# Kernel optimization log

Hardware: AMD Instinct MI355X
Metric: run time of the kernel (lower is better)

## Reference

```python
import jax, jax.numpy as jnp
import numpy as np

D_MODEL = 1024
H = 16
D_K = D_MODEL // H


def setup_inputs() -> dict:
    key = jax.random.key(0)
    ks = jax.random.split(key, 12)
    B, S = 2, 2048
    inp = {
        "q": jax.random.normal(ks[0], (B, S, D_MODEL), jnp.float32),
        "k": jax.random.normal(ks[1], (B, S, D_MODEL), jnp.float32),
        "v": jax.random.normal(ks[2], (B, S, D_MODEL), jnp.float32),
        "mask": jax.random.randint(ks[3], (1, 1, S, S), 0, 2, jnp.int32),
    }
    s = 1.0 / np.sqrt(D_MODEL)
    inp["wq_w"] = jax.random.normal(ks[4], (D_MODEL, D_MODEL), jnp.float32) * s
    inp["wq_b"] = jnp.zeros((D_MODEL,), jnp.float32)
    inp["wk_w"] = jax.random.normal(ks[5], (D_MODEL, D_MODEL), jnp.float32) * s
    inp["wk_b"] = jnp.zeros((D_MODEL,), jnp.float32)
    inp["wv_w"] = jax.random.normal(ks[6], (D_MODEL, D_MODEL), jnp.float32) * s
    inp["wv_b"] = jnp.zeros((D_MODEL,), jnp.float32)
    inp["wo_w"] = jax.random.normal(ks[7], (D_MODEL, D_MODEL), jnp.float32) * s
    inp["wo_b"] = jnp.zeros((D_MODEL,), jnp.float32)
    return inp


def reference(q, k, v, mask, wq_w, wq_b, wk_w, wk_b, wv_w, wv_b, wo_w, wo_b):
    B, S, _ = q.shape
    # projections (torch Linear: x @ W^T + b)
    def proj(x, w, b):
        y = x @ w.T + b
        return y.reshape(B, S, H, D_K).transpose(0, 2, 1, 3)  # [B,H,S,Dk]

    Q = proj(q, wq_w, wq_b)
    K = proj(k, wk_w, wk_b)
    V = proj(v, wv_w, wv_b)

    scores = jnp.einsum("bhqd,bhkd->bhqk", Q, K) / jnp.sqrt(jnp.float32(D_K))
    # source quirk: masked positions set to 1e-9 (NOT -inf) before softmax
    scores = jnp.where(mask == 0, jnp.float32(1e-9), scores)
    attn = jax.nn.softmax(scores, axis=-1)
    out = jnp.einsum("bhqk,bhkd->bhqd", attn, V)
    out = out.transpose(0, 2, 1, 3).reshape(B, S, H * D_K)
    return out @ wo_w.T + wo_b
```

## Files before the change

### kernel.cpp

```cpp
#include <hip/hip_runtime.h>

typedef _Float16 half_t;
typedef _Float16 h8 __attribute__((ext_vector_type(8)));
typedef _Float16 h4 __attribute__((ext_vector_type(4)));
typedef _Float16 h2 __attribute__((ext_vector_type(2)));
typedef float f32x4 __attribute__((ext_vector_type(4)));
typedef float f32x16 __attribute__((ext_vector_type(16)));

#define S_LEN 2048
#define DMODEL 1024
#define NHEAD 16
#define HDK 64
#define NB 2
#define MROWS (NB * S_LEN)
#define LOG2E 1.44269504089f

__device__ __forceinline__ void gload_lds16(const void* g, void* l) {
  __builtin_amdgcn_global_load_lds(
      (const __attribute__((address_space(1))) unsigned int*)g,
      (__attribute__((address_space(3))) unsigned int*)l, 16, 0, 0);
}

__device__ __forceinline__ float fast_exp2(float x) {
  float r;
  asm("v_exp_f32 %0, %1" : "=v"(r) : "v"(x));
  return r;
}

__device__ __forceinline__ int swz(int row, int colByte) {
  return row * 128 + (colByte ^ ((row & 7) << 4));
}

__global__ __launch_bounds__(256) void pre_kernel(
    const float* __restrict__ q, const float* __restrict__ k, const float* __restrict__ v,
    const float* __restrict__ wq, const float* __restrict__ wk,
    const float* __restrict__ wv, const float* __restrict__ wo,
    const int* __restrict__ mask,
    half_t* Xq, half_t* Xk, half_t* Xv,
    half_t* Wq, half_t* Wk, half_t* Wv, half_t* Wo,
    unsigned int* mbits) {
  const int gid = blockIdx.x, tid = threadIdx.x;
  if (gid < 16384) {
    int i = gid * 256 + tid;
    const float* src; half_t* dst; int off;
    if (i < 3145728) {
      int rgn = i >> 20; off = i & 1048575;
      src = rgn == 0 ? q : rgn == 1 ? k : v;
      dst = rgn == 0 ? Xq : rgn == 1 ? Xk : Xv;
    } else {
      int j = i - 3145728;
      int rgn = j >> 18; off = j & 262143;
      src = rgn == 0 ? wq : rgn == 1 ? wk : rgn == 2 ? wv : wo;
      dst = rgn == 0 ? Wq : rgn == 1 ? Wk : rgn == 2 ? Wv : Wo;
    }
    float4 vv = ((const float4*)src)[off];
    h4 o;
    o[0] = (half_t)vv.x; o[1] = (half_t)vv.y; o[2] = (half_t)vv.z; o[3] = (half_t)vv.w;
    ((h4*)dst)[off] = o;
  } else {
    int i = (gid - 16384) * 256 + tid;
    int mv = mask[i];
    unsigned long long bm = __ballot(mv != 0);
    int lane = tid & 63;
    if (lane == 0)       mbits[i >> 5] = (unsigned int)bm;
    else if (lane == 32) mbits[i >> 5] = (unsigned int)(bm >> 32);
  }
}

template <int EPI>
__global__ __launch_bounds__(256) void gemm_kernel(
    const half_t* __restrict__ A0, const half_t* __restrict__ A1, const half_t* __restrict__ A2,
    const half_t* __restrict__ W0, const half_t* __restrict__ W1, const half_t* __restrict__ W2,
    const float* __restrict__ b0, const float* __restrict__ b1, const float* __restrict__ b2,
    void* o0, void* o1, void* o2) {
  const int nwg = gridDim.x;
  const int cpx = nwg >> 3;
  const int id = blockIdx.x;
  const int nid = (id & 7) * cpx + (id >> 3);
  const int z = nid >> 8;
  const int rmn = nid & 255;
  const int bm = rmn >> 3, bn = rmn & 7;

  const half_t* A; const half_t* W; const float* bias; void* out; float scale;
  if (z == 0)      { A = A0; W = W0; bias = b0; out = o0; scale = (EPI == 0) ? 0.125f * LOG2E : 1.0f; }
  else if (z == 1) { A = A1; W = W1; bias = b1; out = o1; scale = 1.0f; }
  else             { A = A2; W = W2; bias = b2; out = o2; scale = 1.0f; }

  __shared__ half_t As[2][128 * 32];
  __shared__ half_t Bs[2][128 * 32];
  const int tid = threadIdx.x;
  const int w = tid >> 6, lane = tid & 63;
  const int wm = w >> 1, wn = w & 1;
  const int crow = lane >> 2;
  const int ckb = ((lane & 3) * 16) ^ ((crow & 3) << 4);

  f32x4 acc[4][4] = {};

  const char* Ar0 = (const char*)A + (size_t)(bm * 128 + w * 16 + crow) * 2048 + ckb;
  const char* Ar1 = Ar0 + 64 * 2048;
  const char* Wr0 = (const char*)W + (size_t)(bn * 128 + w * 16 + crow) * 2048 + ckb;
  const char* Wr1 = Wr0 + 64 * 2048;

  const int rr = lane & 15;
  const int kkB = (lane >> 4) * 16;
  const int kswz = (rr & 3) << 4;

#define GSTAGE(buf, ktB)                                     \
  do {                                                       \
    gload_lds16(Ar0 + (ktB), As[buf] + w * 512);             \
    gload_lds16(Ar1 + (ktB), As[buf] + (w + 4) * 512);       \
    gload_lds16(Wr0 + (ktB), Bs[buf] + w * 512);             \
    gload_lds16(Wr1 + (ktB), Bs[buf] + (w + 4) * 512);       \
  } while (0)

  GSTAGE(0, 0);
  __syncthreads();

  int cur = 0;
  for (int ktB = 0; ktB < 2048; ktB += 64) {
    if (ktB + 64 < 2048) GSTAGE(cur ^ 1, ktB + 64);

    const char* AsB = (const char*)As[cur];
    const char* BsB = (const char*)Bs[cur];
    h8 af[4], bf[4];
#pragma unroll
    for (int i = 0; i < 4; ++i) {
      af[i] = *(const h8*)(AsB + (wm * 64 + i * 16 + rr) * 64 + (kkB ^ kswz));
      bf[i] = *(const h8*)(BsB + (wn * 64 + i * 16 + rr) * 64 + (kkB ^ kswz));
    }
#pragma unroll
    for (int i = 0; i < 4; ++i)
#pragma unroll
      for (int j = 0; j < 4; ++j)
        acc[i][j] = __builtin_amdgcn_mfma_f32_16x16x32_f16(af[i], bf[j], acc[i][j], 0, 0, 0);

    __syncthreads();
    cur ^= 1;
  }
#undef GSTAGE

  const int r0 = bm * 128 + wm * 64;
  const int c0 = bn * 128 + wn * 64;
#pragma unroll
  for (int j = 0; j < 4; ++j) {
    int col = c0 + j * 16 + (lane & 15);
    float bc = bias[col];
#pragma unroll
    for (int i = 0; i < 4; ++i) {
#pragma unroll
      for (int jj = 0; jj < 4; ++jj) {
        int row = r0 + i * 16 + (lane >> 4) * 4 + jj;
        float val = acc[i][j][jj] + bc;
        if (EPI == 0) {
          int bb = row >> 11, s = row & (S_LEN - 1);
          int hh = col >> 6, dk = col & 63;
          if (z == 2) {
            ((half_t*)out)[((size_t)((bb * NHEAD + hh) * HDK + dk)) * S_LEN + s] = (half_t)val;
          } else {
            ((half_t*)out)[(((size_t)(bb * NHEAD + hh)) * S_LEN + s) * HDK + dk] =
                (half_t)(val * scale);
          }
        } else {
          ((float*)out)[(size_t)row * DMODEL + col] = val;
        }
      }
    }
  }
}

__global__ __launch_bounds__(256, 4) void attn_kernel(
    const half_t* __restrict__ Qp, const half_t* __restrict__ Kp,
    const half_t* __restrict__ VTp, const unsigned int* __restrict__ mbits,
    half_t* __restrict__ AO) {
  __shared__ char smem[32768];

  const int tid = threadIdx.x, w = tid >> 6, lane = tid & 63;
  const int qg = w >> 1, kh = w & 1;
  const int id = blockIdx.x;
  const int xcd = id & 7, rest = id >> 3;
  const int bh = (xcd << 2) | (rest >> 5);
  const int qt = rest & 31;
  const int b = bh >> 4, h = bh & 15;
  const int q32 = lane & 31, hi = lane >> 5;
  const int qbase = qt * 64 + qg * 32;
  const half_t* Qb = Qp + (size_t)bh * (S_LEN * HDK);
  const char* Kb = (const char*)(Kp + (size_t)bh * (S_LEN * HDK));
  const char* VTb = (const char*)(VTp + (size_t)bh * (S_LEN * HDK));
  const unsigned int* mrow = mbits + (size_t)(qbase + q32) * (S_LEN / 32);

  char* Ks = smem;
  char* Vs = smem + 16384;
  const int srow = w * 16 + (lane >> 3);
  const int scb = (lane & 7) * 16;

  h8 qf[4];
#pragma unroll
  for (int s = 0; s < 4; ++s)
    qf[s] = *(const h8*)(Qb + (size_t)(qbase + q32) * HDK + s * 16 + hi * 8);

  f32x16 acc0 = {}, acc1 = {};
  float l_run = 0.f;

  unsigned int mw = mrow[kh];
#pragma unroll
  for (int p = 0; p < 2; ++p) {
    int r = srow + p * 8;
    gload_lds16(Kb + (size_t)r * 128 + (scb ^ ((r & 7) << 4)),
                Ks + (w * 16 + p * 8) * 128);
    gload_lds16(VTb + (size_t)r * (S_LEN * 2) + (scb ^ ((r & 7) << 4)),
                Vs + (w * 16 + p * 8) * 128);
  }
  __syncthreads();

  int cur = 0;
  for (int t = 0; t < 32; ++t) {
    const unsigned int mwc = mw >> (hi * 4);

    if (t < 31) {
      const int kvn = t + 1;
#pragma unroll
      for (int p = 0; p < 2; ++p) {
        int r = srow + p * 8;
        gload_lds16(Kb + (size_t)(kvn * 64 + r) * 128 + (scb ^ ((r & 7) << 4)),
                    Ks + (cur ^ 1) * 8192 + (w * 16 + p * 8) * 128);
        gload_lds16(VTb + (size_t)r * (S_LEN * 2) + kvn * 128 + (scb ^ ((r & 7) << 4)),
                    Vs + (cur ^ 1) * 8192 + (w * 16 + p * 8) * 128);
      }
      mw = mrow[kvn * 2 + kh];
    }

    const char* kb = Ks + cur * 8192;
    const char* vb = Vs + cur * 8192;
    f32x16 sc = {};
    __builtin_amdgcn_s_setprio(1);
#pragma unroll
    for (int s = 0; s < 4; ++s) {
      h8 kf = *(const h8*)(kb + swz(kh * 32 + q32, s * 32 + hi * 16));
      sc = __builtin_amdgcn_mfma_f32_32x32x16_f16(kf, qf[s], sc, 0, 0, 0);
    }
    __builtin_amdgcn_s_setprio(0);

    h8 vf00 = *(const h8*)(vb + swz(q32, kh * 64 + hi * 16));
    h8 vf01 = *(const h8*)(vb + swz(q32, kh * 64 + 32 + hi * 16));
    h8 vf10 = *(const h8*)(vb + swz(32 + q32, kh * 64 + hi * 16));
    h8 vf11 = *(const h8*)(vb + swz(32 + q32, kh * 64 + 32 + hi * 16));

#pragma unroll
    for (int rg = 0; rg < 16; ++rg) {
      const int bit = (rg & 3) + 8 * (rg >> 2);
      float p = fast_exp2(((mwc >> bit) & 1u) ? sc[rg] : 0.0f);
      sc[rg] = p;
      l_run += p;
    }

    h8 pb[2];
#pragma unroll
    for (int s = 0; s < 2; ++s) {
      const int rb = s * 8;
      union { h2 h; unsigned int u; } c01, c23, c45, c67;
      c01.h[0] = (half_t)sc[rb + 0]; c01.h[1] = (half_t)sc[rb + 1];
      c23.h[0] = (half_t)sc[rb + 2]; c23.h[1] = (half_t)sc[rb + 3];
      c45.h[0] = (half_t)sc[rb + 4]; c45.h[1] = (half_t)sc[rb + 5];
      c67.h[0] = (half_t)sc[rb + 6]; c67.h[1] = (half_t)sc[rb + 7];
      auto rA = __builtin_amdgcn_permlane32_swap(c01.u, c45.u, false, false);
      auto rB = __builtin_amdgcn_permlane32_swap(c23.u, c67.u, false, false);
      union { unsigned int u[4]; h8 v; } bw;
      bw.u[0] = rA[0]; bw.u[1] = rB[0]; bw.u[2] = rA[1]; bw.u[3] = rB[1];
      pb[s] = bw.v;
    }

    __builtin_amdgcn_s_setprio(1);
    acc0 = __builtin_amdgcn_mfma_f32_32x32x16_f16(vf00, pb[0], acc0, 0, 0, 0);
    acc1 = __builtin_amdgcn_mfma_f32_32x32x16_f16(vf10, pb[0], acc1, 0, 0, 0);
    acc0 = __builtin_amdgcn_mfma_f32_32x32x16_f16(vf01, pb[1], acc0, 0, 0, 0);
    acc1 = __builtin_amdgcn_mfma_f32_32x32x16_f16(vf11, pb[1], acc1, 0, 0, 0);
    __builtin_amdgcn_s_setprio(0);

    __syncthreads();
    cur ^= 1;
  }

  float* my = (float*)smem + (qg * 64 + lane) * 33;
  if (kh) {
#pragma unroll
    for (int rg = 0; rg < 16; ++rg) { my[rg] = acc0[rg]; my[16 + rg] = acc1[rg]; }
    my[32] = l_run;
  }
  __syncthreads();
  if (!kh) {
#pragma unroll
    for (int rg = 0; rg < 16; ++rg) { acc0[rg] += my[rg]; acc1[rg] += my[16 + rg]; }
    l_run += my[32];
    l_run += __shfl_xor(l_run, 32);

    const float inv = 1.0f / l_run;
    const int qrow = qbase + q32;
    half_t* aob = AO + (size_t)(b * S_LEN + qrow) * DMODEL + h * HDK;
#pragma unroll
    for (int rq = 0; rq < 4; ++rq) {
      h4 s0, s1;
#pragma unroll
      for (int j = 0; j < 4; ++j) {
        s0[j] = (half_t)(acc0[rq * 4 + j] * inv);
        s1[j] = (half_t)(acc1[rq * 4 + j] * inv);
      }
      const int d0 = 8 * rq + 4 * hi;
      *(h4*)(aob + d0) = s0;
      *(h4*)(aob + 32 + d0) = s1;
    }
  }
}

extern "C" void kernel_launch(void* const* d_in, const int* in_sizes, int n_in,
                              void* d_out, int out_size, void* d_ws, size_t ws_size,
                              hipStream_t stream) {
  const float* q    = (const float*)d_in[0];
  const float* k    = (const float*)d_in[1];
  const float* v    = (const float*)d_in[2];
  const int*   mask = (const int*)d_in[3];
  const float* wq_w = (const float*)d_in[4];
  const float* wq_b = (const float*)d_in[5];
  const float* wk_w = (const float*)d_in[6];
  const float* wk_b = (const float*)d_in[7];
  const float* wv_w = (const float*)d_in[8];
  const float* wv_b = (const float*)d_in[9];
  const float* wo_w = (const float*)d_in[10];
  const float* wo_b = (const float*)d_in[11];
  float* out = (float*)d_out;

  char* ws = (char*)d_ws;
  const size_t MB = (size_t)1 << 20;
  half_t* Xq = (half_t*)(ws + 0 * MB);
  half_t* Xk = (half_t*)(ws + 8 * MB);
  half_t* Xv = (half_t*)(ws + 16 * MB);
  half_t* Wq = (half_t*)(ws + 24 * MB);
  half_t* Wk = (half_t*)(ws + 26 * MB);
  half_t* Wv = (half_t*)(ws + 28 * MB);
  half_t* Wo = (half_t*)(ws + 30 * MB);
  half_t* Qp = (half_t*)(ws + 32 * MB);
  half_t* Kp = (half_t*)(ws + 40 * MB);
  half_t* VT = (half_t*)(ws + 48 * MB);
  unsigned int* mbits = (unsigned int*)(ws + 56 * MB);
  half_t* AO = Xq;

  pre_kernel<<<32768, 256, 0, stream>>>(q, k, v, wq_w, wk_w, wv_w, wo_w, mask,
                                        Xq, Xk, Xv, Wq, Wk, Wv, Wo, mbits);
  gemm_kernel<0><<<768, 256, 0, stream>>>(
      Xq, Xk, Xv, Wq, Wk, Wv, wq_b, wk_b, wv_b, (void*)Qp, (void*)Kp, (void*)VT);
  attn_kernel<<<1024, 256, 0, stream>>>(Qp, Kp, VT, mbits, AO);
  gemm_kernel<1><<<256, 256, 0, stream>>>(
      AO, AO, AO, Wo, Wo, Wo, wo_b, wo_b, wo_b, (void*)out, (void*)out, (void*)out);

  (void)in_sizes; (void)n_in; (void)out_size; (void)ws_size;
}
```

Baseline: 152.2 us.

## Deepen GEMM and attention pipelines to 4-stage buffers with partial waitcnt barriers

New measurement: 156.5 us. 1.03x slower.

```diff
diff --git a/kernel.cpp b/kernel.cpp
--- a/kernel.cpp
+++ b/kernel.cpp
@@ -12,7 +12,6 @@
 #define NHEAD 16
 #define HDK 64
 #define NB 2
-#define MROWS (NB * S_LEN)
 #define LOG2E 1.44269504089f
 
 __device__ __forceinline__ void gload_lds16(const void* g, void* l) {
@@ -38,7 +37,7 @@
     const int* __restrict__ mask,
     half_t* Xq, half_t* Xk, half_t* Xv,
     half_t* Wq, half_t* Wk, half_t* Wv, half_t* Wo,
-    unsigned int* mbits) {
+    unsigned int* mbT) {
   const int gid = blockIdx.x, tid = threadIdx.x;
   if (gid < 16384) {
     int i = gid * 256 + tid;
@@ -62,13 +61,15 @@
     int mv = mask[i];
     unsigned long long bm = __ballot(mv != 0);
     int lane = tid & 63;
-    if (lane == 0)       mbits[i >> 5] = (unsigned int)bm;
-    else if (lane == 32) mbits[i >> 5] = (unsigned int)(bm >> 32);
+    int widx = ((i >> 5) & 63);
+    int qrow = i >> 11;
+    if (lane == 0)       mbT[widx * S_LEN + qrow] = (unsigned int)bm;
+    else if (lane == 32) mbT[widx * S_LEN + qrow] = (unsigned int)(bm >> 32);
   }
 }
 
 template <int EPI>
-__global__ __launch_bounds__(256) void gemm_kernel(
+__global__ __launch_bounds__(256, 2) void gemm_kernel(
     const half_t* __restrict__ A0, const half_t* __restrict__ A1, const half_t* __restrict__ A2,
     const half_t* __restrict__ W0, const half_t* __restrict__ W1, const half_t* __restrict__ W2,
     const float* __restrict__ b0, const float* __restrict__ b1, const float* __restrict__ b2,
@@ -86,8 +87,8 @@
   else if (z == 1) { A = A1; W = W1; bias = b1; out = o1; scale = 1.0f; }
   else             { A = A2; W = W2; bias = b2; out = o2; scale = 1.0f; }
 
-  __shared__ half_t As[2][128 * 32];
-  __shared__ half_t Bs[2][128 * 32];
+  __shared__ half_t As[4][128 * 32];
+  __shared__ half_t Bs[4][128 * 32];
   const int tid = threadIdx.x;
   const int w = tid >> 6, lane = tid & 63;
   const int wm = w >> 1, wn = w & 1;
@@ -105,39 +106,44 @@
   const int kkB = (lane >> 4) * 16;
   const int kswz = (rr & 3) << 4;
 
-#define GSTAGE(buf, ktB)                                     \
-  do {                                                       \
-    gload_lds16(Ar0 + (ktB), As[buf] + w * 512);             \
-    gload_lds16(Ar1 + (ktB), As[buf] + (w + 4) * 512);       \
-    gload_lds16(Wr0 + (ktB), Bs[buf] + w * 512);             \
-    gload_lds16(Wr1 + (ktB), Bs[buf] + (w + 4) * 512);       \
-  } while (0)
-
-  GSTAGE(0, 0);
-  __syncthreads();
-
-  int cur = 0;
-  for (int ktB = 0; ktB < 2048; ktB += 64) {
-    if (ktB + 64 < 2048) GSTAGE(cur ^ 1, ktB + 64);
-
-    const char* AsB = (const char*)As[cur];
-    const char* BsB = (const char*)Bs[cur];
-    h8 af[4], bf[4];
-#pragma unroll
-    for (int i = 0; i < 4; ++i) {
-      af[i] = *(const h8*)(AsB + (wm * 64 + i * 16 + rr) * 64 + (kkB ^ kswz));
-      bf[i] = *(const h8*)(BsB + (wn * 64 + i * 16 + rr) * 64 + (kkB ^ kswz));
-    }
-#pragma unroll
-    for (int i = 0; i < 4; ++i)
-#pragma unroll
-      for (int j = 0; j < 4; ++j)
-        acc[i][j] = __builtin_amdgcn_mfma_f32_16x16x32_f16(af[i], bf[j], acc[i][j], 0, 0, 0);
-
-    __syncthreads();
-    cur ^= 1;
-  }
-#undef GSTAGE
+#define GS(BUF, T)                                          \
+  { const int ktB_ = (T) * 64;                              \
+    gload_lds16(Ar0 + ktB_, As[BUF] + w * 512);             \
+    gload_lds16(Ar1 + ktB_, As[BUF] + (w + 4) * 512);       \
+    gload_lds16(Wr0 + ktB_, Bs[BUF] + w * 512);             \
+    gload_lds16(Wr1 + ktB_, Bs[BUF] + (w + 4) * 512); }
+
+#define GW                                                  \
+  asm volatile("s_waitcnt vmcnt(8)" ::: "memory");          \
+  __builtin_amdgcn_sched_barrier(0);                        \
+  __builtin_amdgcn_s_barrier();                             \
+  __builtin_amdgcn_sched_barrier(0);
+
+#define GC(BUF)                                                          \
+  { const char* AsB = (const char*)As[BUF];                              \
+    const char* BsB = (const char*)Bs[BUF];                              \
+    h8 af[4], bf[4];                                                     \
+    _Pragma("unroll") for (int i_ = 0; i_ < 4; ++i_) {                   \
+      af[i_] = *(const h8*)(AsB + (wm * 64 + i_ * 16 + rr) * 64 + (kkB ^ kswz)); \
+      bf[i_] = *(const h8*)(BsB + (wn * 64 + i_ * 16 + rr) * 64 + (kkB ^ kswz)); \
+    }                                                                    \
+    __builtin_amdgcn_s_setprio(1);                                       \
+    _Pragma("unroll") for (int i_ = 0; i_ < 4; ++i_)                     \
+      _Pragma("unroll") for (int j_ = 0; j_ < 4; ++j_)                   \
+        acc[i_][j_] = __builtin_amdgcn_mfma_f32_16x16x32_f16(af[i_], bf[j_], acc[i_][j_], 0, 0, 0); \
+    __builtin_amdgcn_s_setprio(0); }
+
+  GS(0, 0); GS(1, 1);
+  for (int g = 0; g < 8; ++g) {
+    const int i0 = g * 4;
+    GS(2, i0 + 2); GW; GC(0);
+    GS(3, i0 + 3); GW; GC(1);
+    { int t2 = i0 + 4; if (t2 > 31) t2 = 31; GS(0, t2); } GW; GC(2);
+    { int t2 = i0 + 5; if (t2 > 31) t2 = 31; GS(1, t2); } GW; GC(3);
+  }
+#undef GS
+#undef GW
+#undef GC
 
   const int r0 = bm * 128 + wm * 64;
   const int c0 = bn * 128 + wn * 64;
@@ -168,11 +174,11 @@
   }
 }
 
-__global__ __launch_bounds__(256, 4) void attn_kernel(
+__global__ __launch_bounds__(256, 2) void attn_kernel(
     const half_t* __restrict__ Qp, const half_t* __restrict__ Kp,
-    const half_t* __restrict__ VTp, const unsigned int* __restrict__ mbits,
+    const half_t* __restrict__ VTp, const unsigned int* __restrict__ mbT,
     half_t* __restrict__ AO) {
-  __shared__ char smem[32768];
+  __shared__ char smem[65536];
 
   const int tid = threadIdx.x, w = tid >> 6, lane = tid & 63;
   const int qg = w >> 1, kh = w & 1;
@@ -186,10 +192,9 @@
   const half_t* Qb = Qp + (size_t)bh * (S_LEN * HDK);
   const char* Kb = (const char*)(Kp + (size_t)bh * (S_LEN * HDK));
   const char* VTb = (const char*)(VTp + (size_t)bh * (S_LEN * HDK));
-  const unsigned int* mrow = mbits + (size_t)(qbase + q32) * (S_LEN / 32);
 
   char* Ks = smem;
-  char* Vs = smem + 16384;
+  char* Vs = smem + 32768;
   const int srow = w * 16 + (lane >> 3);
   const int scb = (lane & 7) * 16;
 
@@ -200,85 +205,85 @@
 
   f32x16 acc0 = {}, acc1 = {};
   float l_run = 0.f;
-
-  unsigned int mw = mrow[kh];
-#pragma unroll
-  for (int p = 0; p < 2; ++p) {
-    int r = srow + p * 8;
-    gload_lds16(Kb + (size_t)r * 128 + (scb ^ ((r & 7) << 4)),
-                Ks + (w * 16 + p * 8) * 128);
-    gload_lds16(VTb + (size_t)r * (S_LEN * 2) + (scb ^ ((r & 7) << 4)),
-                Vs + (w * 16 + p * 8) * 128);
-  }
+  unsigned int mw0s, mw1s, mw2s, mw3s;
+
+#define ASTG(BUF, T)                                                        \
+  { const int t_ = (T);                                                     \
+    _Pragma("unroll") for (int p = 0; p < 2; ++p) {                         \
+      int r = srow + p * 8;                                                 \
+      gload_lds16(Kb + (size_t)(t_ * 64 + r) * 128 + (scb ^ ((r & 7) << 4)),\
+                  Ks + (BUF) * 8192 + (w * 16 + p * 8) * 128);              \
+      gload_lds16(VTb + (size_t)r * (S_LEN * 2) + t_ * 128 + (scb ^ ((r & 7) << 4)), \
+                  Vs + (BUF) * 8192 + (w * 16 + p * 8) * 128);              \
+    } }
+
+#define AMSK(VAR, T) VAR = mbT[(size_t)((T) * 2 + kh) * S_LEN + qbase + q32];
+
+#define AW                                                  \
+  asm volatile("s_waitcnt vmcnt(10)" ::: "memory");         \
+  __builtin_amdgcn_sched_barrier(0);                        \
+  __builtin_amdgcn_s_barrier();                             \
+  __builtin_amdgcn_sched_barrier(0);
+
+#define ABODY(BUF, MW)                                                      \
+  { const char* kb = Ks + (BUF) * 8192;                                     \
+    const char* vb = Vs + (BUF) * 8192;                                     \
+    const unsigned int mwc = (MW) >> (hi * 4);                              \
+    f32x16 sc = {};                                                         \
+    __builtin_amdgcn_s_setprio(1);                                          \
+    _Pragma("unroll") for (int s = 0; s < 4; ++s) {                         \
+      h8 kf = *(const h8*)(kb + swz(kh * 32 + q32, s * 32 + hi * 16));      \
+      sc = __builtin_amdgcn_mfma_f32_32x32x16_f16(kf, qf[s], sc, 0, 0, 0);  \
+    }                                                                       \
+    __builtin_amdgcn_s_setprio(0);                                          \
+    h8 vf00 = *(const h8*)(vb + swz(q32, kh * 64 + hi * 16));               \
+    h8 vf01 = *(const h8*)(vb + swz(q32, kh * 64 + 32 + hi * 16));          \
+    h8 vf10 = *(const h8*)(vb + swz(32 + q32, kh * 64 + hi * 16));          \
+    h8 vf11 = *(const h8*)(vb + swz(32 + q32, kh * 64 + 32 + hi * 16));     \
+    _Pragma("unroll") for (int rg = 0; rg < 16; ++rg) {                     \
+      const int bit = (rg & 3) + 8 * (rg >> 2);                             \
+      float p = fast_exp2(((mwc >> bit) & 1u) ? sc[rg] : 0.0f);             \
+      sc[rg] = p;                                                           \
+      l_run += p;                                                           \
+    }                                                                       \
+    h8 pb[2];                                                               \
+    _Pragma("unroll") for (int s = 0; s < 2; ++s) {                         \
+      const int rb = s * 8;                                                 \
+      union { h2 h_; unsigned int u; } c01, c23, c45, c67;                  \
+      c01.h_[0] = (half_t)sc[rb + 0]; c01.h_[1] = (half_t)sc[rb + 1];       \
+      c23.h_[0] = (half_t)sc[rb + 2]; c23.h_[1] = (half_t)sc[rb + 3];       \
+      c45.h_[0] = (half_t)sc[rb + 4]; c45.h_[1] = (half_t)sc[rb + 5];       \
+      c67.h_[0] = (half_t)sc[rb + 6]; c67.h_[1] = (half_t)sc[rb + 7];       \
+      auto rA = __builtin_amdgcn_permlane32_swap(c01.u, c45.u, false, false);\
+      auto rB = __builtin_amdgcn_permlane32_swap(c23.u, c67.u, false, false);\
+      union { unsigned int u[4]; h8 v_; } bw;                               \
+      bw.u[0] = rA[0]; bw.u[1] = rB[0]; bw.u[2] = rA[1]; bw.u[3] = rB[1];   \
+      pb[s] = bw.v_;                                                        \
+    }                                                                       \
+    __builtin_amdgcn_s_setprio(1);                                          \
+    acc0 = __builtin_amdgcn_mfma_f32_32x32x16_f16(vf00, pb[0], acc0, 0, 0, 0); \
+    acc1 = __builtin_amdgcn_mfma_f32_32x32x16_f16(vf10, pb[0], acc1, 0, 0, 0); \
+    acc0 = __builtin_amdgcn_mfma_f32_32x32x16_f16(vf01, pb[1], acc0, 0, 0, 0); \
+    acc1 = __builtin_amdgcn_mfma_f32_32x32x16_f16(vf11, pb[1], acc1, 0, 0, 0); \
+    __builtin_amdgcn_s_setprio(0); }
+
+  ASTG(0, 0); AMSK(mw0s, 0);
+  ASTG(1, 1); AMSK(mw1s, 1);
+  for (int g = 0; g < 8; ++g) {
+    const int i0 = g * 4;
+    ASTG(2, i0 + 2); AMSK(mw2s, i0 + 2); AW; ABODY(0, mw0s);
+    ASTG(3, i0 + 3); AMSK(mw3s, i0 + 3); AW; ABODY(1, mw1s);
+    { int t2 = i0 + 4; if (t2 > 31) t2 = 31; ASTG(0, t2); AMSK(mw0s, t2); }
+    AW; ABODY(2, mw2s);
+    { int t2 = i0 + 5; if (t2 > 31) t2 = 31; ASTG(1, t2); AMSK(mw1s, t2); }
+    AW; ABODY(3, mw3s);
+  }
+#undef ASTG
+#undef AMSK
+#undef AW
+#undef ABODY
+
   __syncthreads();
-
-  int cur = 0;
-  for (int t = 0; t < 32; ++t) {
-    const unsigned int mwc = mw >> (hi * 4);
-
-    if (t < 31) {
-      const int kvn = t + 1;
-#pragma unroll
-      for (int p = 0; p < 2; ++p) {
-        int r = srow + p * 8;
-        gload_lds16(Kb + (size_t)(kvn * 64 + r) * 128 + (scb ^ ((r & 7) << 4)),
-                    Ks + (cur ^ 1) * 8192 + (w * 16 + p * 8) * 128);
-        gload_lds16(VTb + (size_t)r * (S_LEN * 2) + kvn * 128 + (scb ^ ((r & 7) << 4)),
-                    Vs + (cur ^ 1) * 8192 + (w * 16 + p * 8) * 128);
-      }
-      mw = mrow[kvn * 2 + kh];
-    }
-
-    const char* kb = Ks + cur * 8192;
-    const char* vb = Vs + cur * 8192;
-    f32x16 sc = {};
-    __builtin_amdgcn_s_setprio(1);
-#pragma unroll
-    for (int s = 0; s < 4; ++s) {
-      h8 kf = *(const h8*)(kb + swz(kh * 32 + q32, s * 32 + hi * 16));
-      sc = __builtin_amdgcn_mfma_f32_32x32x16_f16(kf, qf[s], sc, 0, 0, 0);
-    }
-    __builtin_amdgcn_s_setprio(0);
-
-    h8 vf00 = *(const h8*)(vb + swz(q32, kh * 64 + hi * 16));
-    h8 vf01 = *(const h8*)(vb + swz(q32, kh * 64 + 32 + hi * 16));
-    h8 vf10 = *(const h8*)(vb + swz(32 + q32, kh * 64 + hi * 16));
-    h8 vf11 = *(const h8*)(vb + swz(32 + q32, kh * 64 + 32 + hi * 16));
-
-#pragma unroll
-    for (int rg = 0; rg < 16; ++rg) {
-      const int bit = (rg & 3) + 8 * (rg >> 2);
-      float p = fast_exp2(((mwc >> bit) & 1u) ? sc[rg] : 0.0f);
-      sc[rg] = p;
-      l_run += p;
-    }
-
-    h8 pb[2];
-#pragma unroll
-    for (int s = 0; s < 2; ++s) {
-      const int rb = s * 8;
-      union { h2 h; unsigned int u; } c01, c23, c45, c67;
-      c01.h[0] = (half_t)sc[rb + 0]; c01.h[1] = (half_t)sc[rb + 1];
-      c23.h[0] = (half_t)sc[rb + 2]; c23.h[1] = (half_t)sc[rb + 3];
-      c45.h[0] = (half_t)sc[rb + 4]; c45.h[1] = (half_t)sc[rb + 5];
-      c67.h[0] = (half_t)sc[rb + 6]; c67.h[1] = (half_t)sc[rb + 7];
-      auto rA = __builtin_amdgcn_permlane32_swap(c01.u, c45.u, false, false);
-      auto rB = __builtin_amdgcn_permlane32_swap(c23.u, c67.u, false, false);
-      union { unsigned int u[4]; h8 v; } bw;
-      bw.u[0] = rA[0]; bw.u[1] = rB[0]; bw.u[2] = rA[1]; bw.u[3] = rB[1];
-      pb[s] = bw.v;
-    }
-
-    __builtin_amdgcn_s_setprio(1);
-    acc0 = __builtin_amdgcn_mfma_f32_32x32x16_f16(vf00, pb[0], acc0, 0, 0, 0);
-    acc1 = __builtin_amdgcn_mfma_f32_32x32x16_f16(vf10, pb[0], acc1, 0, 0, 0);
-    acc0 = __builtin_amdgcn_mfma_f32_32x32x16_f16(vf01, pb[1], acc0, 0, 0, 0);
-    acc1 = __builtin_amdgcn_mfma_f32_32x32x16_f16(vf11, pb[1], acc1, 0, 0, 0);
-    __builtin_amdgcn_s_setprio(0);
-
-    __syncthreads();
-    cur ^= 1;
-  }
 
   float* my = (float*)smem + (qg * 64 + lane) * 33;
   if (kh) {
@@ -340,14 +345,14 @@
   half_t* Qp = (half_t*)(ws + 32 * MB);
   half_t* Kp = (half_t*)(ws + 40 * MB);
   half_t* VT = (half_t*)(ws + 48 * MB);
-  unsigned int* mbits = (unsigned int*)(ws + 56 * MB);
+  unsigned int* mbT = (unsigned int*)(ws + 56 * MB);
   half_t* AO = Xq;
 
   pre_kernel<<<32768, 256, 0, stream>>>(q, k, v, wq_w, wk_w, wv_w, wo_w, mask,
-                                        Xq, Xk, Xv, Wq, Wk, Wv, Wo, mbits);
+                                        Xq, Xk, Xv, Wq, Wk, Wv, Wo, mbT);
   gemm_kernel<0><<<768, 256, 0, stream>>>(
       Xq, Xk, Xv, Wq, Wk, Wv, wq_b, wk_b, wv_b, (void*)Qp, (void*)Kp, (void*)VT);
-  attn_kernel<<<1024, 256, 0, stream>>>(Qp, Kp, VT, mbits, AO);
+  attn_kernel<<<1024, 256, 0, stream>>>(Qp, Kp, VT, mbT, AO);
   gemm_kernel<1><<<256, 256, 0, stream>>>(
       AO, AO, AO, Wo, Wo, Wo, wo_b, wo_b, wo_b, (void*)out, (void*)out, (void*)out);
 
```
